# Kernel tuning notes

Measured on AMD Instinct MI355X. Metric: run time of the kernel, lower is better.

Reference implementation:

```python
import jax, jax.numpy as jnp
import numpy as np

N = 20000      # total nodes (batched graph)
E = 320000     # total edges
G = 200        # number of graphs in batch
F_IN = 128     # node_feat_dim
HID = 128      # hidden_dim
H = 4          # num_heads
LAT = 128      # latent_dim
O1, O2, O3 = HID // 2, HID, 2 * HID          # per-head out feats of gat1/2/3
D1, D2, D3 = H * O1, H * O2, H * O3          # flattened dims (256, 512, 1024)
NEG_SLOPE = 0.2


def setup_inputs() -> dict:
    key = jax.random.key(0)
    ks = jax.random.split(key, 26)
    nrm = lambda k, shape, fan: jax.random.normal(k, shape, jnp.float32) / np.sqrt(fan)
    inp = {
        "node_feat": jax.random.normal(ks[0], (N, F_IN), jnp.float32),
        "src": jax.random.randint(ks[1], (E,), 0, N),
        "dst": jax.random.randint(ks[2], (E,), 0, N),
        "graph_ids": jnp.sort(jax.random.randint(ks[3], (N,), 0, G)),
        # GAT layer 1
        "W1": nrm(ks[4], (F_IN, D1), F_IN), "al1": nrm(ks[5], (H, O1), O1),
        "ar1": nrm(ks[6], (H, O1), O1), "b1": jnp.zeros((D1,), jnp.float32),
        # GAT layer 2
        "W2": nrm(ks[7], (D1, D2), D1), "al2": nrm(ks[8], (H, O2), O2),
        "ar2": nrm(ks[9], (H, O2), O2), "b2": jnp.zeros((D2,), jnp.float32),
        # GAT layer 3
        "W3": nrm(ks[10], (D2, D3), D2), "al3": nrm(ks[11], (H, O3), O3),
        "ar3": nrm(ks[12], (H, O3), O3), "b3": jnp.zeros((D3,), jnp.float32),
        # gate MLP of GlobalAttentionPooling: Linear(D3,HID)->ReLU->Linear(HID,1)
        "Wg1": nrm(ks[13], (D3, HID), D3), "bg1": jnp.zeros((HID,), jnp.float32),
        "Wg2": nrm(ks[14], (HID, 1), HID), "bg2": jnp.zeros((1,), jnp.float32),
        # latent heads
        "Wmu": nrm(ks[15], (D3, LAT), D3), "bmu": jnp.zeros((LAT,), jnp.float32),
        "Wlv": nrm(ks[16], (D3, LAT), D3), "blv": jnp.zeros((LAT,), jnp.float32),
    }
    return inp


def gat_layer(x, W, al, ar, b, src, dst, out_feat):
    # dgl GATConv: fc -> per-node attn halves -> edge leaky_relu -> segment softmax over dst -> scatter-agg
    feat = (x @ W).reshape(-1, H, out_feat)            # [N,H,O]
    el = jnp.sum(feat * al[None], axis=-1)             # [N,H]
    er = jnp.sum(feat * ar[None], axis=-1)             # [N,H]
    e = jax.nn.leaky_relu(el[src] + er[dst], NEG_SLOPE)  # [E,H]
    emax = jax.ops.segment_max(e, dst, num_segments=N)   # per-dst max (stable softmax)
    ex = jnp.exp(e - emax[dst])                         # [E,H]
    denom = jax.ops.segment_sum(ex, dst, num_segments=N)
    alpha = ex / jnp.maximum(denom[dst], 1e-9)          # [E,H]
    msg = feat[src] * alpha[..., None]                  # [E,H,O]
    rst = jax.ops.segment_sum(msg, dst, num_segments=N)  # [N,H,O] (zero for 0-in-degree)
    return rst.reshape(-1, H * out_feat) + b            # flatten(1) + bias


def reference(node_feat, src, dst, graph_ids,
              W1, al1, ar1, b1, W2, al2, ar2, b2, W3, al3, ar3, b3,
              Wg1, bg1, Wg2, bg2, Wmu, bmu, Wlv, blv):
    h = jax.nn.elu(gat_layer(node_feat, W1, al1, ar1, b1, src, dst, O1))
    h = jax.nn.elu(gat_layer(h, W2, al2, ar2, b2, src, dst, O2))
    h = jax.nn.elu(gat_layer(h, W3, al3, ar3, b3, src, dst, O3))
    # GlobalAttentionPooling: gate MLP -> per-graph softmax over nodes -> weighted sum
    gate = (jax.nn.relu(h @ Wg1 + bg1) @ Wg2 + bg2)[:, 0]          # [N]
    gmax = jax.ops.segment_max(gate, graph_ids, num_segments=G)
    gexp = jnp.exp(gate - gmax[graph_ids])
    gsum = jax.ops.segment_sum(gexp, graph_ids, num_segments=G)
    a = gexp / jnp.maximum(gsum[graph_ids], 1e-9)                  # [N]
    graph_emb = jax.ops.segment_sum(a[:, None] * h, graph_ids, num_segments=G)  # [G,D3]
    return graph_emb @ Wmu + bmu, graph_emb @ Wlv + blv
```

## Files before the change

### kernel.cpp

```cpp
#include <hip/hip_runtime.h>
#include <math.h>

constexpr int N_NODES = 20000;
constexpr int N_EDGES = 320000;
constexpr int N_GRAPH = 200;
constexpr int F_IN    = 128;
constexpr int NH      = 4;
constexpr int O1 = 64,  O2 = 128, O3 = 256;
constexpr int D1 = 256, D2 = 512, D3 = 1024;
constexpr int LAT  = 128;
constexpr int HIDG = 128;
constexpr float NEG_SLOPE = 0.2f;

typedef __attribute__((ext_vector_type(8))) short bf16x8;
typedef __attribute__((ext_vector_type(4))) float f32x4;
typedef __attribute__((ext_vector_type(2))) ushort ushortx2;
typedef __attribute__((ext_vector_type(4))) ushort ushortx4;
typedef __attribute__((ext_vector_type(8))) ushort ushortx8;

template<int R> struct VecU;
template<> struct VecU<2> { using T = ushortx2; };
template<> struct VecU<4> { using T = ushortx4; };
template<> struct VecU<8> { using T = ushortx8; };

__device__ inline void bsplit(float x, ushort& h, ushort& l) {
    unsigned u = __float_as_uint(x);
    unsigned rh = (u + 0x7fffu + ((u >> 16) & 1u)) & 0xffff0000u;
    h = (ushort)(rh >> 16);
    float res = x - __uint_as_float(rh);
    unsigned u2 = __float_as_uint(res);
    l = (ushort)((u2 + 0x7fffu + ((u2 >> 16) & 1u)) >> 16);
}
__device__ inline ushort f2bf(float x) {
    unsigned u = __float_as_uint(x);
    return (ushort)((u + 0x7fffu + ((u >> 16) & 1u)) >> 16);
}
__device__ inline float bf2f(ushort u) { return __uint_as_float(((unsigned)u) << 16); }

__global__ void zero_int(int* __restrict__ p, int n) {
    int i = blockIdx.x * blockDim.x + threadIdx.x;
    if (i < n) p[i] = 0;
}

__global__ void count_deg(const int* __restrict__ dst, int* __restrict__ deg) {
    int e = blockIdx.x * blockDim.x + threadIdx.x;
    if (e < N_EDGES) atomicAdd(&deg[dst[e]], 1);
}

constexpr int SCAN_B = 512;
__global__ __launch_bounds__(SCAN_B)
void scan1(const int* __restrict__ deg, int* __restrict__ rowptr, int* __restrict__ bsum) {
    __shared__ int s[SCAN_B];
    int tid = threadIdx.x;
    int i = blockIdx.x * SCAN_B + tid;
    int v = (i < N_NODES) ? deg[i] : 0;
    s[tid] = v;
    __syncthreads();
    for (int off = 1; off < SCAN_B; off <<= 1) {
        int add = (tid >= off) ? s[tid - off] : 0;
        __syncthreads();
        s[tid] += add;
        __syncthreads();
    }
    if (i < N_NODES) rowptr[i] = s[tid] - v;
    if (tid == SCAN_B - 1) bsum[blockIdx.x] = s[tid];
}

__global__ void scan2(const int* __restrict__ bsum, int* __restrict__ boff, int nblk) {
    if (threadIdx.x == 0 && blockIdx.x == 0) {
        int run = 0;
        for (int b = 0; b < nblk; ++b) { boff[b] = run; run += bsum[b]; }
    }
}

__global__ __launch_bounds__(SCAN_B)
void scan3(int* __restrict__ rowptr, const int* __restrict__ boff, int* __restrict__ pos) {
    int i = blockIdx.x * SCAN_B + threadIdx.x;
    if (i < N_NODES) {
        int v = rowptr[i] + boff[blockIdx.x];
        rowptr[i] = v;
        pos[i] = v;
    }
    if (i == 0) rowptr[N_NODES] = N_EDGES;
}

__global__ void fill_csr(const int* __restrict__ src, const int* __restrict__ dst,
                         int* __restrict__ pos, int* __restrict__ csr_src) {
    int e = blockIdx.x * blockDim.x + threadIdx.x;
    if (e >= N_EDGES) return;
    int slot = atomicAdd(&pos[dst[e]], 1);
    csr_src[slot] = src[e];
}

__global__ void gptr_kernel(const int* __restrict__ gid, int* __restrict__ gptr) {
    int g = blockIdx.x * blockDim.x + threadIdx.x;
    if (g > N_GRAPH) return;
    int lo = 0, hi = N_NODES;
    while (lo < hi) { int mid = (lo + hi) >> 1; if (gid[mid] < g) lo = mid + 1; else hi = mid; }
    gptr[g] = lo;
}

__global__ void split_x(const float* __restrict__ X, ushort* __restrict__ S, int M, int K) {
    int i = blockIdx.x * 256 + threadIdx.x;
    int total = (M * K) >> 2;
    if (i >= total) return;
    int e0 = i << 2;
    int m = e0 / K, k = e0 % K;
    float4 v = *(const float4*)&X[(size_t)m * K + k];
    ushort h[4], l[4];
    bsplit(v.x, h[0], l[0]); bsplit(v.y, h[1], l[1]);
    bsplit(v.z, h[2], l[2]); bsplit(v.w, h[3], l[3]);
    uint2 hp, lp;
    hp.x = (unsigned)h[0] | ((unsigned)h[1] << 16);
    hp.y = (unsigned)h[2] | ((unsigned)h[3] << 16);
    lp.x = (unsigned)l[0] | ((unsigned)l[1] << 16);
    lp.y = (unsigned)l[2] | ((unsigned)l[3] << 16);
    *(uint2*)&S[(size_t)m * 2 * K + k] = hp;
    *(uint2*)&S[(size_t)m * 2 * K + K + k] = lp;
}

__global__ __launch_bounds__(256)
void split_wt(const float* __restrict__ W, ushort* __restrict__ Bt, int K, int N) {
    __shared__ float t[32][33];
    int n0 = blockIdx.x * 32, k0 = blockIdx.y * 32;
    int tx = threadIdx.x, ty = threadIdx.y;
    for (int j = 0; j < 32; j += 8)
        t[ty + j][tx] = W[(size_t)(k0 + ty + j) * N + n0 + tx];
    __syncthreads();
    for (int j = 0; j < 32; j += 8) {
        float v = t[tx][ty + j];
        int n = n0 + ty + j, k = k0 + tx;
        ushort h, l;
        bsplit(v, h, l);
        Bt[(size_t)n * 2 * K + k] = h;
        Bt[(size_t)n * 2 * K + K + k] = l;
    }
}

#define GLOAD_LDS16(g, s) \
    __builtin_amdgcn_global_load_lds((const __attribute__((address_space(1))) void*)(g), \
                                     (__attribute__((address_space(3))) void*)(s), 16, 0, 0)

template<bool BIAS, bool RELU, int OMODE>
__global__ __launch_bounds__(256)
void gemm_mfma(const ushort* __restrict__ Asp, const ushort* __restrict__ Bt,
               const float* __restrict__ bias, void* __restrict__ Cout,
               int M, int N, int K, int ntn, int kchunk) {
    __shared__ __align__(16) ushort lds[4 * 128 * 64];
    constexpr int AH = 0, AL = 128 * 64, BH = 2 * 128 * 64, BL = 3 * 128 * 64;

    const int nwg = gridDim.x;
    int bid = blockIdx.x;
    int q = nwg >> 3, r = nwg & 7;
    int xcd = bid & 7, local = bid >> 3;
    int wg = (xcd < r) ? (xcd * (q + 1) + local) : (r * (q + 1) + (xcd - r) * q + local);
    const int tm = wg / ntn, tn = wg % ntn;

    const int tid = threadIdx.x;
    const int w = tid >> 6, l = tid & 63;
    const int wr = w >> 1, wc = w & 1;
    const size_t sA = 2 * (size_t)K;

    const int ld8 = l >> 3;
    const int stg_col = ((l & 7) ^ ld8) << 3;
    const int r15 = l & 15, kq = l >> 4;
    const int swz = (l & 7) << 4;

    const int k_begin = blockIdx.y * kchunk;
    const int k_end = (k_begin + kchunk < K) ? (k_begin + kchunk) : K;

    f32x4 acc[4][4];
    #pragma unroll
    for (int m = 0; m < 4; ++m)
        #pragma unroll
        for (int n = 0; n < 4; ++n)
            acc[m][n] = 0.f;

    for (int k0 = k_begin; k0 < k_end; k0 += 64) {
        #pragma unroll
        for (int i = 0; i < 4; ++i) {
            int r0 = w * 32 + i * 8;
            int garow = tm * 128 + r0 + ld8;
            if (garow > M - 1) garow = M - 1;
            const ushort* gaH = Asp + (size_t)garow * sA + k0 + stg_col;
            GLOAD_LDS16(gaH, &lds[AH + r0 * 64]);
            GLOAD_LDS16(gaH + K, &lds[AL + r0 * 64]);
            int gbrow = tn * 128 + r0 + ld8;
            const ushort* gbH = Bt + (size_t)gbrow * sA + k0 + stg_col;
            GLOAD_LDS16(gbH, &lds[BH + r0 * 64]);
            GLOAD_LDS16(gbH + K, &lds[BL + r0 * 64]);
        }
        asm volatile("s_waitcnt vmcnt(0)");
        __syncthreads();

        #pragma unroll
        for (int ks = 0; ks < 2; ++ks) {
            const int kbyte = (ks * 64 + kq * 16) ^ swz;
            bf16x8 ah[4], bh[4], xl[4];
            #pragma unroll
            for (int m = 0; m < 4; ++m) {
                int row = wr * 64 + m * 16 + r15;
                ah[m] = *(const bf16x8*)((const char*)&lds[AH] + row * 128 + kbyte);
            }
            #pragma unroll
            for (int n = 0; n < 4; ++n) {
                int row = wc * 64 + n * 16 + r15;
                bh[n] = *(const bf16x8*)((const char*)&lds[BH] + row * 128 + kbyte);
            }
            #pragma unroll
            for (int m = 0; m < 4; ++m)
                #pragma unroll
                for (int n = 0; n < 4; ++n)
                    acc[m][n] = __builtin_amdgcn_mfma_f32_16x16x32_bf16(ah[m], bh[n], acc[m][n], 0, 0, 0);
            #pragma unroll
            for (int m = 0; m < 4; ++m) {
                int row = wr * 64 + m * 16 + r15;
                xl[m] = *(const bf16x8*)((const char*)&lds[AL] + row * 128 + kbyte);
            }
            #pragma unroll
            for (int m = 0; m < 4; ++m)
                #pragma unroll
                for (int n = 0; n < 4; ++n)
                    acc[m][n] = __builtin_amdgcn_mfma_f32_16x16x32_bf16(xl[m], bh[n], acc[m][n], 0, 0, 0);
            #pragma unroll
            for (int n = 0; n < 4; ++n) {
                int row = wc * 64 + n * 16 + r15;
                xl[n] = *(const bf16x8*)((const char*)&lds[BL] + row * 128 + kbyte);
            }
            #pragma unroll
            for (int m = 0; m < 4; ++m)
                #pragma unroll
                for (int n = 0; n < 4; ++n)
                    acc[m][n] = __builtin_amdgcn_mfma_f32_16x16x32_bf16(ah[m], xl[n], acc[m][n], 0, 0, 0);
        }
        __syncthreads();
    }

    #pragma unroll
    for (int m = 0; m < 4; ++m) {
        #pragma unroll
        for (int n = 0; n < 4; ++n) {
            #pragma unroll
            for (int j = 0; j < 4; ++j) {
                int row = tm * 128 + wr * 64 + m * 16 + kq * 4 + j;
                int col = tn * 128 + wc * 64 + n * 16 + r15;
                if (row < M) {
                    float v = acc[m][n][j];
                    if (BIAS) v += bias[col];
                    if (RELU) v = fmaxf(v, 0.f);
                    if (OMODE == 1)
                        ((ushort*)Cout)[(size_t)row * N + col] = f2bf(v);
                    else if (OMODE == 2)
                        ((float*)Cout)[(size_t)blockIdx.y * M * N + (size_t)row * N + col] = v;
                    else
                        ((float*)Cout)[(size_t)row * N + col] = v;
                }
            }
        }
    }
}

__global__ __launch_bounds__(256)
void attn_lr_b(const ushort* __restrict__ feat, const float* __restrict__ al,
               const float* __restrict__ ar, float* __restrict__ el,
               float* __restrict__ er, int O) {
    int n = blockIdx.x;
    int h = threadIdx.x >> 6;
    int lane = threadIdx.x & 63;
    const ushort* fr = feat + (size_t)n * (NH * O) + h * O;
    float sl = 0.f, sr = 0.f;
    for (int o = lane; o < O; o += 64) {
        float f = bf2f(fr[o]);
        sl += f * al[h * O + o];
        sr += f * ar[h * O + o];
    }
    #pragma unroll
    for (int off = 32; off; off >>= 1) {
        sl += __shfl_down(sl, off);
        sr += __shfl_down(sr, off);
    }
    if (lane == 0) {
        el[n * NH + h] = sl;
        er[n * NH + h] = sr;
    }
}

__global__ __launch_bounds__(64)
void attn_softmax(const float* __restrict__ el, const float* __restrict__ er,
                  const int* __restrict__ rowptr, const int* __restrict__ csr_src,
                  float* __restrict__ csr_e, float* __restrict__ rden) {
    int d = blockIdx.x;
    int lane = threadIdx.x;
    int base = rowptr[d], end = rowptr[d + 1];
    float erd[NH];
    #pragma unroll
    for (int h = 0; h < NH; ++h) erd[h] = er[d * NH + h];

    float mx[NH] = {-INFINITY, -INFINITY, -INFINITY, -INFINITY};
    for (int s = base + lane; s < end; s += 64) {
        int sn = csr_src[s];
        #pragma unroll
        for (int h = 0; h < NH; ++h) {
            float v = el[sn * NH + h] + erd[h];
            v = (v >= 0.f) ? v : NEG_SLOPE * v;
            csr_e[s * NH + h] = v;
            mx[h] = fmaxf(mx[h], v);
        }
    }
    #pragma unroll
    for (int h = 0; h < NH; ++h)
        #pragma unroll
        for (int off = 32; off; off >>= 1)
            mx[h] = fmaxf(mx[h], __shfl_xor(mx[h], off));

    float sm[NH] = {0.f, 0.f, 0.f, 0.f};
    for (int s = base + lane; s < end; s += 64) {
        #pragma unroll
        for (int h = 0; h < NH; ++h) {
            float ex = expf(csr_e[s * NH + h] - mx[h]);
            csr_e[s * NH + h] = ex;
            sm[h] += ex;
        }
    }
    #pragma unroll
    for (int h = 0; h < NH; ++h)
        #pragma unroll
        for (int off = 32; off; off >>= 1)
            sm[h] += __shfl_xor(sm[h], off);

    if (lane == 0) {
        #pragma unroll
        for (int h = 0; h < NH; ++h)
            rden[d * NH + h] = 1.f / fmaxf(sm[h], 1e-9f);
    }
}

template<int REGS, int OSHIFT>
__global__ __launch_bounds__(128)
void aggregate_b(const ushort* __restrict__ feat, const float* __restrict__ csr_e,
                 const float* __restrict__ rden, const int* __restrict__ rowptr,
                 const int* __restrict__ csr_src, const float* __restrict__ bias,
                 ushort* __restrict__ Ssp, int D) {
    using VT = typename VecU<REGS>::T;
    int d = blockIdx.x;
    int t = threadIdx.x;
    int base = rowptr[d], end = rowptr[d + 1];
    const int col0 = t * REGS;
    const int h = col0 >> OSHIFT;

    float acc[REGS];
    #pragma unroll
    for (int k = 0; k < REGS; ++k) acc[k] = 0.f;

    int s = base;
    for (; s + 3 < end; s += 4) {
        int sn0 = csr_src[s], sn1 = csr_src[s + 1];
        int sn2 = csr_src[s + 2], sn3 = csr_src[s + 3];
        float a0 = csr_e[s * NH + h],       a1 = csr_e[(s + 1) * NH + h];
        float a2 = csr_e[(s + 2) * NH + h], a3 = csr_e[(s + 3) * NH + h];
        VT u0 = *(const VT*)(feat + (size_t)sn0 * D + col0);
        VT u1 = *(const VT*)(feat + (size_t)sn1 * D + col0);
        VT u2 = *(const VT*)(feat + (size_t)sn2 * D + col0);
        VT u3 = *(const VT*)(feat + (size_t)sn3 * D + col0);
        #pragma unroll
        for (int k = 0; k < REGS; ++k) acc[k] += bf2f(u0[k]) * a0;
        #pragma unroll
        for (int k = 0; k < REGS; ++k) acc[k] += bf2f(u1[k]) * a1;
        #pragma unroll
        for (int k = 0; k < REGS; ++k) acc[k] += bf2f(u2[k]) * a2;
        #pragma unroll
        for (int k = 0; k < REGS; ++k) acc[k] += bf2f(u3[k]) * a3;
    }
    if (s + 1 < end) {
        int sn0 = csr_src[s], sn1 = csr_src[s + 1];
        float a0 = csr_e[s * NH + h], a1 = csr_e[(s + 1) * NH + h];
        VT u0 = *(const VT*)(feat + (size_t)sn0 * D + col0);
        VT u1 = *(const VT*)(feat + (size_t)sn1 * D + col0);
        #pragma unroll
        for (int k = 0; k < REGS; ++k) acc[k] += bf2f(u0[k]) * a0;
        #pragma unroll
        for (int k = 0; k < REGS; ++k) acc[k] += bf2f(u1[k]) * a1;
        s += 2;
    }
    if (s < end) {
        int sn = csr_src[s];
        float a = csr_e[s * NH + h];
        VT u = *(const VT*)(feat + (size_t)sn * D + col0);
        #pragma unroll
        for (int k = 0; k < REGS; ++k) acc[k] += bf2f(u[k]) * a;
    }

    float rd = rden[d * NH + h];
    ushort hh[REGS], ll[REGS];
    #pragma unroll
    for (int k = 0; k < REGS; ++k) {
        float v = acc[k] * rd + bias[col0 + k];
        v = (v > 0.f) ? v : expm1f(v);
        bsplit(v, hh[k], ll[k]);
    }
    ushort* hrow = Ssp + (size_t)d * 2 * D;
    #pragma unroll
    for (int k = 0; k < REGS; ++k) {
        hrow[col0 + k] = hh[k];
        hrow[D + col0 + k] = ll[k];
    }
}

__global__ __launch_bounds__(128)
void gate_reduce(const float* __restrict__ part, const float* __restrict__ bg1,
                 const float* __restrict__ Wg2, const float* __restrict__ bg2,
                 float* __restrict__ gate) {
    int n = blockIdx.x;
    int t = threadIdx.x;
    constexpr size_t CH = (size_t)N_NODES * HIDG;
    size_t idx = (size_t)n * HIDG + t;
    float v = part[idx] + part[CH + idx] + part[2 * CH + idx] + part[3 * CH + idx] + bg1[t];
    v = fmaxf(v, 0.f) * Wg2[t];
    __shared__ float red[128];
    red[t] = v;
    __syncthreads();
    for (int s = 64; s; s >>= 1) {
        if (t < s) red[t] += red[t + s];
        __syncthreads();
    }
    if (t == 0) gate[n] = red[0] + bg2[0];
}

__global__ __launch_bounds__(64)
void gate_stats(const float* __restrict__ gate, const int* __restrict__ gptr,
                float* __restrict__ anorm) {
    int g = blockIdx.x;
    int lane = threadIdx.x;
    int s = gptr[g], e = gptr[g + 1];
    float m = -INFINITY;
    for (int n = s + lane; n < e; n += 64) m = fmaxf(m, gate[n]);
    #pragma unroll
    for (int off = 32; off; off >>= 1) m = fmaxf(m, __shfl_xor(m, off));
    float sum = 0.f;
    for (int n = s + lane; n < e; n += 64) sum += expf(gate[n] - m);
    #pragma unroll
    for (int off = 32; off; off >>= 1) sum += __shfl_xor(sum, off);
    float inv = 1.f / fmaxf(sum, 1e-9f);
    for (int n = s + lane; n < e; n += 64) anorm[n] = expf(gate[n] - m) * inv;
}

__global__ __launch_bounds__(256)
void pool_gather(const ushort* __restrict__ h3sp, const float* __restrict__ anorm,
                 const int* __restrict__ gptr, float* __restrict__ gemb) {
    int g = blockIdx.y;
    int col = (blockIdx.x * 256 + threadIdx.x) * 2;
    float acc0 = 0.f, acc1 = 0.f;
    int s = gptr[g], e = gptr[g + 1];
    int n = s;
    for (; n + 3 < e; n += 4) {
        const ushort* r0 = h3sp + (size_t)(n + 0) * 2 * D3;
        const ushort* r1 = h3sp + (size_t)(n + 1) * 2 * D3;
        const ushort* r2 = h3sp + (size_t)(n + 2) * 2 * D3;
        const ushort* r3 = h3sp + (size_t)(n + 3) * 2 * D3;
        float a0 = anorm[n], a1 = anorm[n + 1], a2 = anorm[n + 2], a3 = anorm[n + 3];
        ushortx2 h0 = *(const ushortx2*)(r0 + col), l0 = *(const ushortx2*)(r0 + D3 + col);
        ushortx2 h1 = *(const ushortx2*)(r1 + col), l1 = *(const ushortx2*)(r1 + D3 + col);
        ushortx2 h2 = *(const ushortx2*)(r2 + col), l2 = *(const ushortx2*)(r2 + D3 + col);
        ushortx2 h3 = *(const ushortx2*)(r3 + col), l3 = *(const ushortx2*)(r3 + D3 + col);
        acc0 += a0 * (bf2f(h0[0]) + bf2f(l0[0])); acc1 += a0 * (bf2f(h0[1]) + bf2f(l0[1]));
        acc0 += a1 * (bf2f(h1[0]) + bf2f(l1[0])); acc1 += a1 * (bf2f(h1[1]) + bf2f(l1[1]));
        acc0 += a2 * (bf2f(h2[0]) + bf2f(l2[0])); acc1 += a2 * (bf2f(h2[1]) + bf2f(l2[1]));
        acc0 += a3 * (bf2f(h3[0]) + bf2f(l3[0])); acc1 += a3 * (bf2f(h3[1]) + bf2f(l3[1]));
    }
    for (; n < e; ++n) {
        const ushort* r0 = h3sp + (size_t)n * 2 * D3;
        float a0 = anorm[n];
        ushortx2 h0 = *(const ushortx2*)(r0 + col), l0 = *(const ushortx2*)(r0 + D3 + col);
        acc0 += a0 * (bf2f(h0[0]) + bf2f(l0[0]));
        acc1 += a0 * (bf2f(h0[1]) + bf2f(l0[1]));
    }
    gemb[(size_t)g * D3 + col] = acc0;
    gemb[(size_t)g * D3 + col + 1] = acc1;
}

__global__ __launch_bounds__(128)
void heads_kernel(const float* __restrict__ gemb, const float* __restrict__ Wmu,
                  const float* __restrict__ bmu, const float* __restrict__ Wlv,
                  const float* __restrict__ blv, float* __restrict__ out) {
    int g = blockIdx.x;
    int j = threadIdx.x;
    __shared__ float e[D3];
    for (int k = threadIdx.x; k < D3; k += 128) e[k] = gemb[(size_t)g * D3 + k];
    __syncthreads();
    float smu = 0.f, slv = 0.f;
    for (int k = 0; k < D3; ++k) {
        float v = e[k];
        smu += v * Wmu[k * LAT + j];
        slv += v * Wlv[k * LAT + j];
    }
    out[g * LAT + j] = smu + bmu[j];
    out[N_GRAPH * LAT + g * LAT + j] = slv + blv[j];
}

extern "C" void kernel_launch(void* const* d_in, const int* in_sizes, int n_in,
                              void* d_out, int out_size, void* d_ws, size_t ws_size,
                              hipStream_t stream) {
    const float* node_feat = (const float*)d_in[0];
    const int*   src = (const int*)d_in[1];
    const int*   dst = (const int*)d_in[2];
    const int*   gid = (const int*)d_in[3];
    const float* W1  = (const float*)d_in[4];
    const float* al1 = (const float*)d_in[5];
    const float* ar1 = (const float*)d_in[6];
    const float* b1  = (const float*)d_in[7];
    const float* W2  = (const float*)d_in[8];
    const float* al2 = (const float*)d_in[9];
    const float* ar2 = (const float*)d_in[10];
    const float* b2  = (const float*)d_in[11];
    const float* W3  = (const float*)d_in[12];
    const float* al3 = (const float*)d_in[13];
    const float* ar3 = (const float*)d_in[14];
    const float* b3  = (const float*)d_in[15];
    const float* Wg1 = (const float*)d_in[16];
    const float* bg1 = (const float*)d_in[17];
    const float* Wg2 = (const float*)d_in[18];
    const float* bg2 = (const float*)d_in[19];
    const float* Wmu = (const float*)d_in[20];
    const float* bmu = (const float*)d_in[21];
    const float* Wlv = (const float*)d_in[22];
    const float* blv = (const float*)d_in[23];
    float* out = (float*)d_out;

    char* wsb = (char*)d_ws;
    float* bufA   = (float*)wsb;
    wsb += (size_t)N_NODES * D3 * 4;
    ushort* Xsp   = (ushort*)wsb;
    wsb += (size_t)N_NODES * 2048 * 2;
    ushort* Bt1   = (ushort*)wsb; wsb += (size_t)D1 * 2 * F_IN * 2;
    ushort* Bt2   = (ushort*)wsb; wsb += (size_t)D2 * 2 * D1 * 2;
    ushort* Bt3   = (ushort*)wsb; wsb += (size_t)D3 * 2 * D2 * 2;
    ushort* Btg   = (ushort*)wsb; wsb += (size_t)HIDG * 2 * D3 * 2;
    float* el     = (float*)wsb;  wsb += (size_t)N_NODES * NH * 4;
    float* er     = (float*)wsb;  wsb += (size_t)N_NODES * NH * 4;
    float* rden   = (float*)wsb;  wsb += (size_t)N_NODES * NH * 4;
    float* csr_e  = (float*)wsb;  wsb += (size_t)N_EDGES * NH * 4;
    float* gate   = (float*)wsb;  wsb += (size_t)N_NODES * 4;
    float* anorm  = (float*)wsb;  wsb += (size_t)N_NODES * 4;
    int* deg      = (int*)wsb;    wsb += (size_t)N_NODES * 4;
    int* rowptr   = (int*)wsb;    wsb += (size_t)(N_NODES + 1) * 4;
    int* pos      = (int*)wsb;    wsb += (size_t)N_NODES * 4;
    int* csr_src  = (int*)wsb;    wsb += (size_t)N_EDGES * 4;
    int* bsum     = (int*)wsb;    wsb += 64 * 4;
    int* boff     = (int*)wsb;    wsb += 64 * 4;
    int* gptr     = (int*)wsb;    wsb += (size_t)(N_GRAPH + 1) * 4;
    ushort* featb = (ushort*)bufA;
    float* partial = bufA;
    float* gemb   = bufA + (size_t)4 * N_NODES * HIDG;

    constexpr int NBLK = (N_NODES + SCAN_B - 1) / SCAN_B;
    zero_int<<<dim3((N_NODES + 255) / 256), dim3(256), 0, stream>>>(deg, N_NODES);
    count_deg<<<dim3((N_EDGES + 255) / 256), dim3(256), 0, stream>>>(dst, deg);
    scan1<<<dim3(NBLK), dim3(SCAN_B), 0, stream>>>(deg, rowptr, bsum);
    scan2<<<dim3(1), dim3(64), 0, stream>>>(bsum, boff, NBLK);
    scan3<<<dim3(NBLK), dim3(SCAN_B), 0, stream>>>(rowptr, boff, pos);
    fill_csr<<<dim3((N_EDGES + 255) / 256), dim3(256), 0, stream>>>(src, dst, pos, csr_src);
    gptr_kernel<<<dim3(1), dim3(256), 0, stream>>>(gid, gptr);

    split_wt<<<dim3(D1 / 32, F_IN / 32), dim3(32, 8), 0, stream>>>(W1, Bt1, F_IN, D1);
    split_wt<<<dim3(D2 / 32, D1 / 32),   dim3(32, 8), 0, stream>>>(W2, Bt2, D1, D2);
    split_wt<<<dim3(D3 / 32, D2 / 32),   dim3(32, 8), 0, stream>>>(W3, Bt3, D2, D3);
    split_wt<<<dim3(HIDG / 32, D3 / 32), dim3(32, 8), 0, stream>>>(Wg1, Btg, D3, HIDG);

    split_x<<<dim3((N_NODES * F_IN / 4 + 255) / 256), dim3(256), 0, stream>>>(node_feat, Xsp, N_NODES, F_IN);

    gemm_mfma<false, false, 1><<<dim3(157 * 2), dim3(256), 0, stream>>>(Xsp, Bt1, nullptr, featb, N_NODES, D1, F_IN, 2, F_IN);
    attn_lr_b<<<dim3(N_NODES), dim3(256), 0, stream>>>(featb, al1, ar1, el, er, O1);
    attn_softmax<<<dim3(N_NODES), dim3(64), 0, stream>>>(el, er, rowptr, csr_src, csr_e, rden);
    aggregate_b<2, 6><<<dim3(N_NODES), dim3(128), 0, stream>>>(featb, csr_e, rden, rowptr, csr_src, b1, Xsp, D1);

    gemm_mfma<false, false, 1><<<dim3(157 * 4), dim3(256), 0, stream>>>(Xsp, Bt2, nullptr, featb, N_NODES, D2, D1, 4, D1);
    attn_lr_b<<<dim3(N_NODES), dim3(256), 0, stream>>>(featb, al2, ar2, el, er, O2);
    attn_softmax<<<dim3(N_NODES), dim3(64), 0, stream>>>(el, er, rowptr, csr_src, csr_e, rden);
    aggregate_b<4, 7><<<dim3(N_NODES), dim3(128), 0, stream>>>(featb, csr_e, rden, rowptr, csr_src, b2, Xsp, D2);

    gemm_mfma<false, false, 1><<<dim3(157 * 8), dim3(256), 0, stream>>>(Xsp, Bt3, nullptr, featb, N_NODES, D3, D2, 8, D2);
    attn_lr_b<<<dim3(N_NODES), dim3(256), 0, stream>>>(featb, al3, ar3, el, er, O3);
    attn_softmax<<<dim3(N_NODES), dim3(64), 0, stream>>>(el, er, rowptr, csr_src, csr_e, rden);
    aggregate_b<8, 8><<<dim3(N_NODES), dim3(128), 0, stream>>>(featb, csr_e, rden, rowptr, csr_src, b3, Xsp, D3);

    gemm_mfma<false, false, 2><<<dim3(157, 4), dim3(256), 0, stream>>>(Xsp, Btg, nullptr, partial, N_NODES, HIDG, D3, 1, D3 / 4);
    gate_reduce<<<dim3(N_NODES), dim3(128), 0, stream>>>(partial, bg1, Wg2, bg2, gate);
    gate_stats<<<dim3(N_GRAPH), dim3(64), 0, stream>>>(gate, gptr, anorm);
    pool_gather<<<dim3(D3 / 512, N_GRAPH), dim3(256), 0, stream>>>(Xsp, anorm, gptr, gemb);
    heads_kernel<<<dim3(N_GRAPH), dim3(128), 0, stream>>>(gemb, Wmu, bmu, Wlv, blv, out);
}
```

Measured before the change: 529.1 us.

## Store edge scores head-major, split layer-3 aggregation, widen pooling and heads grids

Edge attention scores are now stored head-major ([H][E]) so aggregation reads them as contiguous float4 vectors alongside int4 loads of source indices, with a scalar prologue that aligns to four edges. The layer-3 aggregation is split across two column blocks per node with four registers per thread, doubling the block count and lowering per-thread register use. pool_gather uses smaller 64-thread blocks over more column tiles for more parallelism. heads_kernel runs the mu and logvar heads on separate thread halves. The trade-off is that softmax writes are now strided by head, and the layer-3 split gathers each node's neighbour indices and scores twice.

```diff
diff --git a/kernel.cpp b/kernel.cpp
--- a/kernel.cpp
+++ b/kernel.cpp
@@ -288,7 +288,7 @@
 __global__ __launch_bounds__(64)
 void attn_softmax(const float* __restrict__ el, const float* __restrict__ er,
                   const int* __restrict__ rowptr, const int* __restrict__ csr_src,
-                  float* __restrict__ csr_e, float* __restrict__ rden) {
+                  float* __restrict__ csrE, float* __restrict__ rden) {
     int d = blockIdx.x;
     int lane = threadIdx.x;
     int base = rowptr[d], end = rowptr[d + 1];
@@ -303,7 +303,7 @@
         for (int h = 0; h < NH; ++h) {
             float v = el[sn * NH + h] + erd[h];
             v = (v >= 0.f) ? v : NEG_SLOPE * v;
-            csr_e[s * NH + h] = v;
+            csrE[(size_t)h * N_EDGES + s] = v;
             mx[h] = fmaxf(mx[h], v);
         }
     }
@@ -317,8 +317,8 @@
     for (int s = base + lane; s < end; s += 64) {
         #pragma unroll
         for (int h = 0; h < NH; ++h) {
-            float ex = expf(csr_e[s * NH + h] - mx[h]);
-            csr_e[s * NH + h] = ex;
+            float ex = expf(csrE[(size_t)h * N_EDGES + s] - mx[h]);
+            csrE[(size_t)h * N_EDGES + s] = ex;
             sm[h] += ex;
         }
     }
@@ -335,9 +335,9 @@
     }
 }
 
-template<int REGS, int OSHIFT>
+template<int REGS, int OSHIFT, int CS>
 __global__ __launch_bounds__(128)
-void aggregate_b(const ushort* __restrict__ feat, const float* __restrict__ csr_e,
+void aggregate_b(const ushort* __restrict__ feat, const float* __restrict__ csrE,
                  const float* __restrict__ rden, const int* __restrict__ rowptr,
                  const int* __restrict__ csr_src, const float* __restrict__ bias,
                  ushort* __restrict__ Ssp, int D) {
@@ -345,46 +345,41 @@
     int d = blockIdx.x;
     int t = threadIdx.x;
     int base = rowptr[d], end = rowptr[d + 1];
-    const int col0 = t * REGS;
+    const int col0 = blockIdx.y * (128 * REGS) + t * REGS;
     const int h = col0 >> OSHIFT;
+    const float* eh = csrE + (size_t)h * N_EDGES;
 
     float acc[REGS];
     #pragma unroll
     for (int k = 0; k < REGS; ++k) acc[k] = 0.f;
 
     int s = base;
+    for (; s < end && (s & 3); ++s) {
+        int sn = csr_src[s];
+        float a = eh[s];
+        VT u = *(const VT*)(feat + (size_t)sn * D + col0);
+        #pragma unroll
+        for (int k = 0; k < REGS; ++k) acc[k] += bf2f(u[k]) * a;
+    }
     for (; s + 3 < end; s += 4) {
-        int sn0 = csr_src[s], sn1 = csr_src[s + 1];
-        int sn2 = csr_src[s + 2], sn3 = csr_src[s + 3];
-        float a0 = csr_e[s * NH + h],       a1 = csr_e[(s + 1) * NH + h];
-        float a2 = csr_e[(s + 2) * NH + h], a3 = csr_e[(s + 3) * NH + h];
-        VT u0 = *(const VT*)(feat + (size_t)sn0 * D + col0);
-        VT u1 = *(const VT*)(feat + (size_t)sn1 * D + col0);
-        VT u2 = *(const VT*)(feat + (size_t)sn2 * D + col0);
-        VT u3 = *(const VT*)(feat + (size_t)sn3 * D + col0);
-        #pragma unroll
-        for (int k = 0; k < REGS; ++k) acc[k] += bf2f(u0[k]) * a0;
-        #pragma unroll
-        for (int k = 0; k < REGS; ++k) acc[k] += bf2f(u1[k]) * a1;
-        #pragma unroll
-        for (int k = 0; k < REGS; ++k) acc[k] += bf2f(u2[k]) * a2;
-        #pragma unroll
-        for (int k = 0; k < REGS; ++k) acc[k] += bf2f(u3[k]) * a3;
-    }
-    if (s + 1 < end) {
-        int sn0 = csr_src[s], sn1 = csr_src[s + 1];
-        float a0 = csr_e[s * NH + h], a1 = csr_e[(s + 1) * NH + h];
-        VT u0 = *(const VT*)(feat + (size_t)sn0 * D + col0);
-        VT u1 = *(const VT*)(feat + (size_t)sn1 * D + col0);
-        #pragma unroll
-        for (int k = 0; k < REGS; ++k) acc[k] += bf2f(u0[k]) * a0;
-        #pragma unroll
-        for (int k = 0; k < REGS; ++k) acc[k] += bf2f(u1[k]) * a1;
-        s += 2;
-    }
-    if (s < end) {
+        int4 sn = *(const int4*)(csr_src + s);
+        float4 av = *(const float4*)(eh + s);
+        VT u0 = *(const VT*)(feat + (size_t)sn.x * D + col0);
+        VT u1 = *(const VT*)(feat + (size_t)sn.y * D + col0);
+        VT u2 = *(const VT*)(feat + (size_t)sn.z * D + col0);
+        VT u3 = *(const VT*)(feat + (size_t)sn.w * D + col0);
+        #pragma unroll
+        for (int k = 0; k < REGS; ++k) acc[k] += bf2f(u0[k]) * av.x;
+        #pragma unroll
+        for (int k = 0; k < REGS; ++k) acc[k] += bf2f(u1[k]) * av.y;
+        #pragma unroll
+        for (int k = 0; k < REGS; ++k) acc[k] += bf2f(u2[k]) * av.z;
+        #pragma unroll
+        for (int k = 0; k < REGS; ++k) acc[k] += bf2f(u3[k]) * av.w;
+    }
+    for (; s < end; ++s) {
         int sn = csr_src[s];
-        float a = csr_e[s * NH + h];
+        float a = eh[s];
         VT u = *(const VT*)(feat + (size_t)sn * D + col0);
         #pragma unroll
         for (int k = 0; k < REGS; ++k) acc[k] += bf2f(u[k]) * a;
@@ -444,11 +439,11 @@
     for (int n = s + lane; n < e; n += 64) anorm[n] = expf(gate[n] - m) * inv;
 }
 
-__global__ __launch_bounds__(256)
+__global__ __launch_bounds__(64)
 void pool_gather(const ushort* __restrict__ h3sp, const float* __restrict__ anorm,
                  const int* __restrict__ gptr, float* __restrict__ gemb) {
     int g = blockIdx.y;
-    int col = (blockIdx.x * 256 + threadIdx.x) * 2;
+    int col = blockIdx.x * 128 + threadIdx.x * 2;
     float acc0 = 0.f, acc1 = 0.f;
     int s = gptr[g], e = gptr[g + 1];
     int n = s;
@@ -478,23 +473,23 @@
     gemb[(size_t)g * D3 + col + 1] = acc1;
 }
 
-__global__ __launch_bounds__(128)
+__global__ __launch_bounds__(256)
 void heads_kernel(const float* __restrict__ gemb, const float* __restrict__ Wmu,
                   const float* __restrict__ bmu, const float* __restrict__ Wlv,
                   const float* __restrict__ blv, float* __restrict__ out) {
     int g = blockIdx.x;
-    int j = threadIdx.x;
+    int t = threadIdx.x;
+    int j = t & 127;
+    bool lv = t >= 128;
     __shared__ float e[D3];
-    for (int k = threadIdx.x; k < D3; k += 128) e[k] = gemb[(size_t)g * D3 + k];
+    for (int k = t; k < D3; k += 256) e[k] = gemb[(size_t)g * D3 + k];
     __syncthreads();
-    float smu = 0.f, slv = 0.f;
-    for (int k = 0; k < D3; ++k) {
-        float v = e[k];
-        smu += v * Wmu[k * LAT + j];
-        slv += v * Wlv[k * LAT + j];
-    }
-    out[g * LAT + j] = smu + bmu[j];
-    out[N_GRAPH * LAT + g * LAT + j] = slv + blv[j];
+    const float* W = lv ? Wlv : Wmu;
+    float s = 0.f;
+    #pragma unroll 4
+    for (int k = 0; k < D3; ++k) s += e[k] * W[(size_t)k * LAT + j];
+    s += (lv ? blv : bmu)[j];
+    out[(lv ? (size_t)N_GRAPH * LAT : 0) + (size_t)g * LAT + j] = s;
 }
 
 extern "C" void kernel_launch(void* const* d_in, const int* in_sizes, int n_in,
@@ -538,7 +533,7 @@
     float* el     = (float*)wsb;  wsb += (size_t)N_NODES * NH * 4;
     float* er     = (float*)wsb;  wsb += (size_t)N_NODES * NH * 4;
     float* rden   = (float*)wsb;  wsb += (size_t)N_NODES * NH * 4;
-    float* csr_e  = (float*)wsb;  wsb += (size_t)N_EDGES * NH * 4;
+    float* csrE   = (float*)wsb;  wsb += (size_t)N_EDGES * NH * 4;
     float* gate   = (float*)wsb;  wsb += (size_t)N_NODES * 4;
     float* anorm  = (float*)wsb;  wsb += (size_t)N_NODES * 4;
     int* deg      = (int*)wsb;    wsb += (size_t)N_NODES * 4;
@@ -570,22 +565,22 @@
 
     gemm_mfma<false, false, 1><<<dim3(157 * 2), dim3(256), 0, stream>>>(Xsp, Bt1, nullptr, featb, N_NODES, D1, F_IN, 2, F_IN);
     attn_lr_b<<<dim3(N_NODES), dim3(256), 0, stream>>>(featb, al1, ar1, el, er, O1);
-    attn_softmax<<<dim3(N_NODES), dim3(64), 0, stream>>>(el, er, rowptr, csr_src, csr_e, rden);
-    aggregate_b<2, 6><<<dim3(N_NODES), dim3(128), 0, stream>>>(featb, csr_e, rden, rowptr, csr_src, b1, Xsp, D1);
+    attn_softmax<<<dim3(N_NODES), dim3(64), 0, stream>>>(el, er, rowptr, csr_src, csrE, rden);
+    aggregate_b<2, 6, 1><<<dim3(N_NODES, 1), dim3(128), 0, stream>>>(featb, csrE, rden, rowptr, csr_src, b1, Xsp, D1);
 
     gemm_mfma<false, false, 1><<<dim3(157 * 4), dim3(256), 0, stream>>>(Xsp, Bt2, nullptr, featb, N_NODES, D2, D1, 4, D1);
     attn_lr_b<<<dim3(N_NODES), dim3(256), 0, stream>>>(featb, al2, ar2, el, er, O2);
-    attn_softmax<<<dim3(N_NODES), dim3(64), 0, stream>>>(el, er, rowptr, csr_src, csr_e, rden);
-    aggregate_b<4, 7><<<dim3(N_NODES), dim3(128), 0, stream>>>(featb, csr_e, rden, rowptr, csr_src, b2, Xsp, D2);
+    attn_softmax<<<dim3(N_NODES), dim3(64), 0, stream>>>(el, er, rowptr, csr_src, csrE, rden);
+    aggregate_b<4, 7, 1><<<dim3(N_NODES, 1), dim3(128), 0, stream>>>(featb, csrE, rden, rowptr, csr_src, b2, Xsp, D2);
 
     gemm_mfma<false, false, 1><<<dim3(157 * 8), dim3(256), 0, stream>>>(Xsp, Bt3, nullptr, featb, N_NODES, D3, D2, 8, D2);
     attn_lr_b<<<dim3(N_NODES), dim3(256), 0, stream>>>(featb, al3, ar3, el, er, O3);
-    attn_softmax<<<dim3(N_NODES), dim3(64), 0, stream>>>(el, er, rowptr, csr_src, csr_e, rden);
-    aggregate_b<8, 8><<<dim3(N_NODES), dim3(128), 0, stream>>>(featb, csr_e, rden, rowptr, csr_src, b3, Xsp, D3);
+    attn_softmax<<<dim3(N_NODES), dim3(64), 0, stream>>>(el, er, rowptr, csr_src, csrE, rden);
+    aggregate_b<4, 8, 2><<<dim3(N_NODES, 2), dim3(128), 0, stream>>>(featb, csrE, rden, rowptr, csr_src, b3, Xsp, D3);
 
     gemm_mfma<false, false, 2><<<dim3(157, 4), dim3(256), 0, stream>>>(Xsp, Btg, nullptr, partial, N_NODES, HIDG, D3, 1, D3 / 4);
     gate_reduce<<<dim3(N_NODES), dim3(128), 0, stream>>>(partial, bg1, Wg2, bg2, gate);
     gate_stats<<<dim3(N_GRAPH), dim3(64), 0, stream>>>(gate, gptr, anorm);
-    pool_gather<<<dim3(D3 / 512, N_GRAPH), dim3(256), 0, stream>>>(Xsp, anorm, gptr, gemb);
-    heads_kernel<<<dim3(N_GRAPH), dim3(128), 0, stream>>>(gemb, Wmu, bmu, Wlv, blv, out);
-}
+    pool_gather<<<dim3(D3 / 128, N_GRAPH), dim3(64), 0, stream>>>(Xsp, anorm, gptr, gemb);
+    heads_kernel<<<dim3(N_GRAPH), dim3(256), 0, stream>>>(gemb, Wmu, bmu, Wlv, blv, out);
+}
```

After: 551.4 us. 1.04x slower.
